# Kernel tuning notes

Measured on AMD Instinct MI355X. Metric: run time of the kernel, lower is better.

The kernel has to match this reference:

```python
import jax, jax.numpy as jnp
import numpy as np

DIM = 128
HEADS = 4
KV_RANK = 64
Q_RANK = 32
ROPE = DIM // 2   # 64
NOPE = DIM // 2   # 64
VDIM = DIM // 2   # 64
B, H, W = 2, 64, 64
EPS = 1e-5


def _conv1x1(x, w, b):
    # x: [B,C,H,W], w: [O,C], b: [O]
    return jnp.einsum('bchw,oc->bohw', x, w) + b[None, :, None, None]


def _gn1(x, g, b):
    # GroupNorm with 1 group: normalize over (C,H,W) per sample
    mu = jnp.mean(x, axis=(1, 2, 3), keepdims=True)
    var = jnp.mean((x - mu) ** 2, axis=(1, 2, 3), keepdims=True)
    return (x - mu) / jnp.sqrt(var + EPS) * g[None, :, None, None] + b[None, :, None, None]


def _freqs(h, w):
    # Replicates RotaryPositionalEncoding: pe[...,0::4]=sin_h, 1::4=cos_h, 2::4=sin_w, 3::4=cos_w
    n = ROPE // 4
    inv = 1.0 / (10000.0 ** (jnp.arange(n, dtype=jnp.float32) / n))
    ah = jnp.arange(h, dtype=jnp.float32)[:, None] * inv  # [h,n]
    aw = jnp.arange(w, dtype=jnp.float32)[:, None] * inv  # [w,n]
    fh = jnp.stack([jnp.sin(ah), jnp.cos(ah)], -1)  # [h,n,2] -> (real=sin_h, imag=cos_h)
    fw = jnp.stack([jnp.sin(aw), jnp.cos(aw)], -1)  # [w,n,2]
    fh_b = jnp.broadcast_to(fh[:, None], (h, w, n, 2))
    fw_b = jnp.broadcast_to(fw[None, :], (h, w, n, 2))
    # interleave pairs: pair 2m -> fh[m], pair 2m+1 -> fw[m]
    pe = jnp.stack([fh_b, fw_b], axis=3).reshape(h * w, ROPE // 2, 2)
    return pe  # [S, ROPE//2, 2]


def _rope(x, f):
    # x: [..., S, ROPE]; f: [S, ROPE//2, 2]
    xp = x.reshape(x.shape[:-1] + (ROPE // 2, 2))
    fr, fi = f[..., 0], f[..., 1]  # [S, ROPE//2] broadcast over leading dims
    rr = xp[..., 0] * fr - xp[..., 1] * fi
    ri = xp[..., 0] * fi + xp[..., 1] * fr
    return jnp.stack([rr, ri], -1).reshape(x.shape)


def setup_inputs() -> dict:
    key = jax.random.key(0)
    ks = jax.random.split(key, 8)
    s = 0.02
    inp = {
        'x': jax.random.normal(ks[0], (B, DIM, H, W), dtype=jnp.float32),
        'q1_w': jax.random.normal(ks[1], (Q_RANK, DIM), dtype=jnp.float32) * s,
        'q1_b': jnp.zeros((Q_RANK,), jnp.float32),
        'q_gn_g': jnp.ones((Q_RANK,), jnp.float32),
        'q_gn_b': jnp.zeros((Q_RANK,), jnp.float32),
        'q2_w': jax.random.normal(ks[2], (HEADS * (NOPE + ROPE), Q_RANK), dtype=jnp.float32) * s,
        'q2_b': jnp.zeros((HEADS * (NOPE + ROPE),), jnp.float32),
        'kv1_w': jax.random.normal(ks[3], (KV_RANK + ROPE, DIM), dtype=jnp.float32) * s,
        'kv1_b': jnp.zeros((KV_RANK + ROPE,), jnp.float32),
        'kv_gn_g': jnp.ones((KV_RANK + ROPE,), jnp.float32),
        'kv_gn_b': jnp.zeros((KV_RANK + ROPE,), jnp.float32),
        'kvn_g': jnp.ones((KV_RANK,), jnp.float32),
        'kvn_b': jnp.zeros((KV_RANK,), jnp.float32),
        'kvup_w': jax.random.normal(ks[4], (HEADS * (NOPE + VDIM), KV_RANK), dtype=jnp.float32) * s,
        'kvup_b': jnp.zeros((HEADS * (NOPE + VDIM),), jnp.float32),
        'out_w': jax.random.normal(ks[5], (DIM, HEADS * VDIM), dtype=jnp.float32) * s,
        'out_b': jnp.zeros((DIM,), jnp.float32),
    }
    return inp


def reference(x, q1_w, q1_b, q_gn_g, q_gn_b, q2_w, q2_b, kv1_w, kv1_b, kv_gn_g, kv_gn_b, kvn_g, kvn_b, kvup_w, kvup_b, out_w, out_b):
    b, c, h, w = x.shape
    s = h * w
    f = _freqs(h, w)  # [S, ROPE//2, 2]

    # Q path: low-rank down -> GN -> up
    q = _conv1x1(_gn1(_conv1x1(x, q1_w, q1_b), q_gn_g, q_gn_b), q2_w, q2_b)
    q = q.reshape(b, HEADS, NOPE + ROPE, s).transpose(0, 1, 3, 2)  # [B,H,S,D]
    q_nope, q_rope = q[..., :NOPE], q[..., NOPE:]
    q = jnp.concatenate([q_nope, _rope(q_rope, f)], axis=-1)

    # KV path: joint down-proj, split rope-k and compressed kv
    kv = _gn1(_conv1x1(x, kv1_w, kv1_b), kv_gn_g, kv_gn_b)  # [B, ROPE+KV_RANK, H, W]
    k_rope_c, kv_c = kv[:, :ROPE], kv[:, ROPE:]
    kv_u = _conv1x1(_gn1(kv_c, kvn_g, kvn_b), kvup_w, kvup_b)
    kv_u = kv_u.reshape(b, HEADS, NOPE + VDIM, s).transpose(0, 1, 3, 2)
    k_nope, v = kv_u[..., :NOPE], kv_u[..., NOPE:]

    k_rope = _rope(k_rope_c.reshape(b, ROPE, s).transpose(0, 2, 1)[:, None], f)  # [B,1,S,ROPE]
    k = jnp.concatenate([k_nope, jnp.broadcast_to(k_rope, (b, HEADS, s, ROPE))], axis=-1)

    scale = (NOPE + ROPE) ** -0.5
    attn = jax.nn.softmax(jnp.einsum('bhqd,bhkd->bhqk', q, k) * scale, axis=-1)
    o = jnp.einsum('bhqk,bhkd->bhqd', attn, v)  # [B,H,S,VDIM]
    o = o.transpose(0, 1, 3, 2).reshape(b, HEADS * VDIM, h, w)
    return _conv1x1(o, out_w, out_b) + x
```

## Files before the change

kernel.cpp:

```cpp
#include <hip/hip_runtime.h>

typedef unsigned short ushort_t;
typedef unsigned int uint_t;
typedef __attribute__((ext_vector_type(8))) short s16x8;
typedef __attribute__((ext_vector_type(4))) short s16x4;
typedef __attribute__((ext_vector_type(4))) float f32x4;
typedef __attribute__((ext_vector_type(16))) float f32x16;

#define S_TOT 4096
#define QSCALE 0.08838834764831845f
#define LOG2E 1.4426950408889634f
#define QSL (QSCALE * LOG2E)
#define L2_10000_D16 0.8304820237218406f

__device__ __forceinline__ ushort_t f2b(float f) {
  uint_t u = __float_as_uint(f);
  uint_t r = (u + 0x7FFFu + ((u >> 16) & 1u)) >> 16;
  return (ushort_t)r;
}

__device__ __forceinline__ float b2f(ushort_t u) {
  return __uint_as_float((uint_t)u << 16);
}

__device__ __forceinline__ uint_t cvt_pk_bf16(float lo, float hi) {
  uint_t r;
  asm("v_cvt_pk_bf16_f32 %0, %1, %2" : "=v"(r) : "v"(lo), "v"(hi));
  return r;
}

__device__ __forceinline__ void gload16(const void* g, void* l) {
  __builtin_amdgcn_global_load_lds(
      (const __attribute__((address_space(1))) unsigned int*)g,
      (__attribute__((address_space(3))) unsigned int*)l, 16, 0, 0);
}

__device__ __forceinline__ void rope_pair(float& x0, float& x1, int p, int hi, int wi, float scale) {
  float inv = exp2f(-(float)(p >> 1) * L2_10000_D16);
  float ang = ((p & 1) ? (float)wi : (float)hi) * inv;
  float sn = sinf(ang), cs = cosf(ang);
  float r0 = (x0 * sn - x1 * cs) * scale;
  float r1 = (x0 * cs + x1 * sn) * scale;
  x0 = r0; x1 = r1;
}

__global__ __launch_bounds__(256) void k_conv1(
    const float* __restrict__ x, const float* __restrict__ q1_w, const float* __restrict__ q1_b,
    const float* __restrict__ kv1_w, const float* __restrict__ kv1_b,
    float* __restrict__ y_q, float* __restrict__ y_kv, double* __restrict__ pch,
    const float* __restrict__ q2_w, const float* __restrict__ kvup_w,
    const float* __restrict__ out_w, ushort_t* __restrict__ wq2,
    ushort_t* __restrict__ wkvup, ushort_t* __restrict__ wout) {
  if (blockIdx.x >= 512) {
    int i = (blockIdx.x - 512) * 256 + threadIdx.x;
    if (i < 16384) wq2[i] = f2b(q2_w[i]);
    else if (i < 49152) wkvup[i - 16384] = f2b(kvup_w[i - 16384]);
    else if (i < 81920) wout[i - 49152] = f2b(out_w[i - 49152]);
    return;
  }
  const int b = blockIdx.x >> 8, blk = blockIdx.x & 255, st = blk * 16;
  const int t = threadIdx.x, si = t & 15, g = t >> 4;
  __shared__ float xs[128][16];
#pragma unroll
  for (int i = 0; i < 8; i++) {
    int c = g + 16 * i;
    xs[c][si] = x[(size_t)(b * 128 + c) * S_TOT + st + si];
  }
  __syncthreads();
  float acc[10];
#pragma unroll
  for (int i = 0; i < 10; i++) {
    int oc = g * 10 + i;
    acc[i] = (oc < 32) ? q1_b[oc] : kv1_b[oc - 32];
  }
  const float4* q1w4 = (const float4*)q1_w;
  const float4* kv1w4 = (const float4*)kv1_w;
  for (int c4 = 0; c4 < 32; c4++) {
    float x0 = xs[c4 * 4 + 0][si], x1 = xs[c4 * 4 + 1][si];
    float x2 = xs[c4 * 4 + 2][si], x3 = xs[c4 * 4 + 3][si];
#pragma unroll
    for (int i = 0; i < 10; i++) {
      int oc = g * 10 + i;
      float4 wv = (oc < 32) ? q1w4[oc * 32 + c4] : kv1w4[(oc - 32) * 32 + c4];
      acc[i] += wv.x * x0 + wv.y * x1 + wv.z * x2 + wv.w * x3;
    }
  }
  double* pbase = pch + (size_t)(b * 256 + blk) * 320;
#pragma unroll
  for (int i = 0; i < 10; i++) {
    int oc = g * 10 + i;
    float a = acc[i];
    if (oc < 32) y_q[(size_t)(b * 32 + oc) * S_TOT + st + si] = a;
    else         y_kv[(size_t)(b * 128 + oc - 32) * S_TOT + st + si] = a;
    double s = a, q = (double)a * a;
#pragma unroll
    for (int o = 1; o < 16; o <<= 1) { s += __shfl_xor(s, o, 16); q += __shfl_xor(q, o, 16); }
    if (si == 0) { pbase[oc * 2] = s; pbase[oc * 2 + 1] = q; }
  }
}

__global__ __launch_bounds__(256) void k_red(
    const double* __restrict__ pch, double* __restrict__ SQ) {
  const int pair = blockIdx.x;
  const int b = pair / 160, c = pair % 160;
  const int tid = threadIdx.x;
  __shared__ double rs[256], rq[256];
  rs[tid] = pch[(size_t)(b * 256 + tid) * 320 + c * 2];
  rq[tid] = pch[(size_t)(b * 256 + tid) * 320 + c * 2 + 1];
  __syncthreads();
#pragma unroll
  for (int o = 128; o > 0; o >>= 1) {
    if (tid < o) { rs[tid] += rs[tid + o]; rq[tid] += rq[tid + o]; }
    __syncthreads();
  }
  if (tid == 0) { SQ[pair * 2] = rs[0]; SQ[pair * 2 + 1] = rq[0]; }
}

__global__ __launch_bounds__(512) void k_stats(
    const double* __restrict__ SQ,
    const float* __restrict__ qg, const float* __restrict__ qb,
    const float* __restrict__ kvg, const float* __restrict__ kvb,
    const float* __restrict__ kng, const float* __restrict__ knb,
    float* __restrict__ coef) {
  __shared__ double Sh[2][160], Qh[2][160];
  const int tid = threadIdx.x;
  if (tid < 320) {
    int b = tid / 160, c = tid % 160;
    Sh[b][c] = SQ[tid * 2]; Qh[b][c] = SQ[tid * 2 + 1];
  }
  __syncthreads();
  if (tid < 2) {
    int b = tid;
    float* cf = coef + b * 320;
    const double NS = 4096.0;
    double muq = 0, m2q = 0;
    for (int c = 0; c < 32; c++) { muq += Sh[b][c]; m2q += Qh[b][c]; }
    muq /= (32.0 * NS); m2q /= (32.0 * NS);
    double rstdq = 1.0 / sqrt(m2q - muq * muq + 1e-5);
    for (int c = 0; c < 32; c++) {
      double A = rstdq * (double)qg[c];
      cf[c] = (float)A; cf[32 + c] = (float)((double)qb[c] - muq * A);
    }
    double mukv = 0, m2kv = 0;
    for (int c = 0; c < 128; c++) { mukv += Sh[b][32 + c]; m2kv += Qh[b][32 + c]; }
    mukv /= (128.0 * NS); m2kv /= (128.0 * NS);
    double rstdkv = 1.0 / sqrt(m2kv - mukv * mukv + 1e-5);
    for (int c = 0; c < 64; c++) {
      double A = rstdkv * (double)kvg[c];
      cf[64 + c] = (float)A; cf[128 + c] = (float)((double)kvb[c] - mukv * A);
    }
    double mu2 = 0, m22 = 0;
    for (int c2 = 0; c2 < 64; c2++) {
      int c = 64 + c2;
      double a = rstdkv * (double)kvg[c], bb = (double)kvb[c] - mukv * a;
      double Ec = Sh[b][32 + c] / NS, M2c = Qh[b][32 + c] / NS;
      mu2 += a * Ec + bb;
      m22 += a * a * M2c + 2.0 * a * bb * Ec + bb * bb;
    }
    mu2 /= 64.0; m22 /= 64.0;
    double rstd2 = 1.0 / sqrt(m22 - mu2 * mu2 + 1e-5);
    for (int c2 = 0; c2 < 64; c2++) {
      int c = 64 + c2;
      double a = rstdkv * (double)kvg[c], bb = (double)kvb[c] - mukv * a;
      cf[192 + c2] = (float)(a * rstd2 * (double)kng[c2]);
      cf[256 + c2] = (float)((bb - mu2) * rstd2 * (double)kng[c2] + (double)knb[c2]);
    }
  }
}

__global__ __launch_bounds__(256) void k_gq(
    const float* __restrict__ y_q, const float* __restrict__ coef,
    const ushort_t* __restrict__ wq2, const float* __restrict__ q2_b,
    ushort_t* __restrict__ Q) {
  const int id = blockIdx.x;
  const int h = id & 3, st = (id >> 2) & 63, b = id >> 8;
  const int t = threadIdx.x, si = t & 63, wid = t >> 6;
  const int l15 = t & 15, lg = (t >> 4) & 3;
  const float* cf = coef + b * 320;
  __shared__ __align__(16) ushort_t Xt[64][64];
  __shared__ __align__(16) ushort_t sQ[64][128];
  {
    ushort_t pk[8];
#pragma unroll
    for (int j = 0; j < 8; j++) {
      int c = wid * 8 + j;
      float v = y_q[(size_t)(b * 32 + c) * S_TOT + st * 64 + si];
      pk[j] = f2b(v * cf[c] + cf[32 + c]);
    }
    *(s16x8*)((char*)&Xt[si][0] + ((wid * 16) ^ ((si & 7) << 4))) = *(s16x8*)pk;
  }
  __syncthreads();
  const int d0w = wid * 32;
  f32x4 acc[2][4];
#pragma unroll
  for (int db = 0; db < 2; db++) {
    f32x4 bv;
#pragma unroll
    for (int r = 0; r < 4; r++) bv[r] = q2_b[h * 128 + d0w + db * 16 + lg * 4 + r];
#pragma unroll
    for (int sb = 0; sb < 4; sb++) acc[db][sb] = bv;
  }
  s16x8 wf[2];
#pragma unroll
  for (int db = 0; db < 2; db++)
    wf[db] = *(const s16x8*)(wq2 + (size_t)(h * 128 + d0w + db * 16 + l15) * 32 + lg * 8);
  const int xsw = (lg * 16) ^ ((l15 & 7) << 4);
#pragma unroll
  for (int sb = 0; sb < 4; sb++) {
    s16x8 xf = *(const s16x8*)((const char*)&Xt[sb * 16 + l15][0] + xsw);
#pragma unroll
    for (int db = 0; db < 2; db++)
      acc[db][sb] = __builtin_amdgcn_mfma_f32_16x16x32_bf16(wf[db], xf, acc[db][sb], 0, 0, 0);
  }
  if (wid >= 2) {
#pragma unroll
    for (int db = 0; db < 2; db++)
#pragma unroll
      for (int sb = 0; sb < 4; sb++) {
        int sp = st * 64 + sb * 16 + l15, hi = sp >> 6, wi = sp & 63;
        int dg = d0w + db * 16 + lg * 4;
#pragma unroll
        for (int pr = 0; pr < 2; pr++) {
          float v0 = acc[db][sb][pr * 2], v1 = acc[db][sb][pr * 2 + 1];
          int p = (dg + pr * 2 - 64) >> 1;
          rope_pair(v0, v1, p, hi, wi, QSL);
          acc[db][sb][pr * 2] = v0; acc[db][sb][pr * 2 + 1] = v1;
        }
      }
  } else {
#pragma unroll
    for (int db = 0; db < 2; db++)
#pragma unroll
      for (int sb = 0; sb < 4; sb++)
#pragma unroll
        for (int r = 0; r < 4; r++) acc[db][sb][r] *= QSL;
  }
#pragma unroll
  for (int db = 0; db < 2; db++)
#pragma unroll
    for (int sb = 0; sb < 4; sb++) {
      ushort_t pk[4];
#pragma unroll
      for (int r = 0; r < 4; r++) pk[r] = f2b(acc[db][sb][r]);
      int srow = sb * 16 + l15;
      *(s16x4*)((char*)&sQ[srow][0] + (((d0w + db * 16 + lg * 4) * 2) ^ ((srow & 7) << 4))) =
          *(s16x4*)pk;
    }
  __syncthreads();
  ushort_t* qrow = Q + ((size_t)(b * 4 + h) * S_TOT + st * 64 + si) * 128 + wid * 32;
#pragma unroll
  for (int j = 0; j < 4; j++) {
    s16x8 v = *(const s16x8*)((const char*)&sQ[si][0] + ((wid * 64 + j * 16) ^ ((si & 7) << 4)));
    *(s16x8*)(qrow + j * 8) = v;
  }
}

__global__ __launch_bounds__(256) void k_gkv(
    const float* __restrict__ y_kv, const float* __restrict__ coef,
    const ushort_t* __restrict__ wkvup, const float* __restrict__ kvup_b,
    ushort_t* __restrict__ K, ushort_t* __restrict__ VT) {
  const int id = blockIdx.x;
  const int h = id & 3, st = (id >> 2) & 63, b = id >> 8;
  const int t = threadIdx.x, si = t & 63, wid = t >> 6;
  const int l15 = t & 15, lg = (t >> 4) & 3;
  const float* cf = coef + b * 320;
  __shared__ __align__(16) ushort_t Xt[64][64];
  __shared__ __align__(16) ushort_t sK[64][64];
  {
#pragma unroll
    for (int half = 0; half < 2; half++) {
      ushort_t pk[8];
#pragma unroll
      for (int j = 0; j < 8; j++) {
        int c2 = wid * 16 + half * 8 + j;
        float v = y_kv[(size_t)(b * 128 + 64 + c2) * S_TOT + st * 64 + si];
        pk[j] = f2b(v * cf[192 + c2] + cf[256 + c2]);
      }
      *(s16x8*)((char*)&Xt[si][0] + ((wid * 32 + half * 16) ^ ((si & 7) << 4))) = *(s16x8*)pk;
    }
  }
  __syncthreads();
  const int d0w = wid * 32;
  f32x4 acc[2][4];
#pragma unroll
  for (int db = 0; db < 2; db++) {
    f32x4 bv;
#pragma unroll
    for (int r = 0; r < 4; r++) bv[r] = kvup_b[h * 128 + d0w + db * 16 + lg * 4 + r];
#pragma unroll
    for (int sb = 0; sb < 4; sb++) acc[db][sb] = bv;
  }
  s16x8 wf[2][2];
#pragma unroll
  for (int db = 0; db < 2; db++)
#pragma unroll
    for (int kk = 0; kk < 2; kk++)
      wf[db][kk] = *(const s16x8*)(wkvup + (size_t)(h * 128 + d0w + db * 16 + l15) * 64 +
                                   kk * 32 + lg * 8);
#pragma unroll
  for (int sb = 0; sb < 4; sb++) {
#pragma unroll
    for (int kk = 0; kk < 2; kk++) {
      s16x8 xf = *(const s16x8*)((const char*)&Xt[sb * 16 + l15][0] +
                                 ((kk * 64 + lg * 16) ^ ((l15 & 7) << 4)));
#pragma unroll
      for (int db = 0; db < 2; db++)
        acc[db][sb] = __builtin_amdgcn_mfma_f32_16x16x32_bf16(wf[db][kk], xf, acc[db][sb], 0, 0, 0);
    }
  }
  if (wid < 2) {
#pragma unroll
    for (int db = 0; db < 2; db++)
#pragma unroll
      for (int sb = 0; sb < 4; sb++) {
        ushort_t pk[4];
#pragma unroll
        for (int r = 0; r < 4; r++) pk[r] = f2b(acc[db][sb][r]);
        int srow = sb * 16 + l15;
        *(s16x4*)((char*)&sK[srow][0] + (((d0w + db * 16 + lg * 4) * 2) ^ ((srow & 7) << 4))) =
            *(s16x4*)pk;
      }
  } else {
    ushort_t* vb = VT + (size_t)(b * 4 + h) * 64 * S_TOT;
#pragma unroll
    for (int db = 0; db < 2; db++)
#pragma unroll
      for (int sb = 0; sb < 4; sb++) {
        int sp = st * 64 + sb * 16 + l15;
#pragma unroll
        for (int r = 0; r < 4; r++) {
          int vd = (wid - 2) * 32 + db * 16 + lg * 4 + r;
          vb[(size_t)vd * S_TOT + sp] = f2b(acc[db][sb][r]);
        }
      }
  }
  __syncthreads();
  const int sp = st * 64 + si;
  ushort_t* krow = K + ((size_t)(b * 4 + h) * S_TOT + sp) * 128;
#pragma unroll
  for (int j = 0; j < 2; j++) {
    s16x8 v = *(const s16x8*)((const char*)&sK[si][0] + ((wid * 32 + j * 16) ^ ((si & 7) << 4)));
    *(s16x8*)(krow + wid * 16 + j * 8) = v;
  }
  {
    const int c0 = wid * 16, hi = sp >> 6, wi = sp & 63;
    float v[16];
#pragma unroll
    for (int j = 0; j < 16; j++) {
      int c = c0 + j;
      v[j] = y_kv[(size_t)(b * 128 + c) * S_TOT + sp] * cf[64 + c] + cf[128 + c];
    }
#pragma unroll
    for (int k = 0; k < 8; k++) {
      int p = (c0 >> 1) + k;
      rope_pair(v[2 * k], v[2 * k + 1], p, hi, wi, 1.0f);
    }
    ushort_t pk[16];
#pragma unroll
    for (int j = 0; j < 16; j++) pk[j] = f2b(v[j]);
    *(s16x8*)(krow + 64 + c0) = *(s16x8*)pk;
    *(s16x8*)(krow + 64 + c0 + 8) = *(s16x8*)(pk + 8);
  }
}

__global__ __launch_bounds__(256, 3) void k_attn(
    const ushort_t* __restrict__ Q, const ushort_t* __restrict__ K,
    const ushort_t* __restrict__ VT, ushort_t* __restrict__ Opart,
    float* __restrict__ ml) {
  const int bid = blockIdx.x;
  const int bh = bid & 7;
  const int rest = bid >> 3;
  const int half = rest >> 5, qblk = rest & 31;
  const int kv0 = half * 2048;
  const int tid = threadIdx.x;
  const int wid = tid >> 6, lane = tid & 63;
  const int l31 = lane & 31, hi = lane >> 5;
  const int qbase = qblk * 128 + wid * 32;
  const ushort_t* Qp = Q + (size_t)bh * S_TOT * 128;
  const ushort_t* Kp = K + (size_t)bh * S_TOT * 128;
  const ushort_t* Vp = VT + (size_t)bh * 64 * S_TOT;

  __shared__ __align__(16) ushort_t K_lds[2][64][128];
  __shared__ __align__(16) ushort_t V_lds[2][64][64];

  s16x8 qf[8];
#pragma unroll
  for (int c = 0; c < 8; c++)
    qf[c] = *(const s16x8*)(Qp + (size_t)(qbase + l31) * 128 + c * 16 + hi * 8);

  f32x16 o0, o1;
#pragma unroll
  for (int r = 0; r < 16; r++) { o0[r] = 0.f; o1[r] = 0.f; }
  float m_s = -1e30f, l_s = 0.f;

  const int krow_l = tid >> 4;
  const int kcolb = (tid & 15) * 16;
  const int vrow_l = tid >> 3;
  const int vcolb = (tid & 7) * 16;

#define STAGE(kvb, bufi)                                                          \
  {                                                                               \
    _Pragma("unroll")                                                             \
    for (int i = 0; i < 4; i++) {                                                 \
      int row = i * 16 + krow_l;                                                  \
      int colb = kcolb ^ ((row & 15) << 4);                                       \
      gload16((const char*)(Kp + (size_t)((kvb) + row) * 128) + colb,             \
              (void*)&K_lds[bufi][i * 16 + wid * 4][0]);                          \
    }                                                                             \
    _Pragma("unroll")                                                             \
    for (int i = 0; i < 2; i++) {                                                 \
      int vd = i * 32 + vrow_l;                                                   \
      int colb = vcolb ^ ((vd & 7) << 4);                                         \
      gload16((const char*)(Vp + (size_t)vd * S_TOT + (kvb)) + colb,              \
              (void*)&V_lds[bufi][i * 32 + wid * 8][0]);                          \
    }                                                                             \
  }

  STAGE(kv0, 0);
  __syncthreads();

  const int kswz = (l31 & 15) << 4;
  const int vswz = (l31 & 7) << 4;
#pragma unroll 1
  for (int t = 0; t < 32; t++) {
    const int buf = t & 1;
    if (t < 31) STAGE(kv0 + (t + 1) * 64, buf ^ 1);
    f32x16 sc0, sc1;
#pragma unroll
    for (int r = 0; r < 16; r++) { sc0[r] = 0.f; sc1[r] = 0.f; }
    __builtin_amdgcn_s_setprio(1);
#pragma unroll
    for (int c = 0; c < 8; c++) {
      const int off = (c * 32 + hi * 16) ^ kswz;
      s16x8 k0 = *(const s16x8*)((const char*)&K_lds[buf][l31][0] + off);
      s16x8 k1 = *(const s16x8*)((const char*)&K_lds[buf][32 + l31][0] + off);
      sc0 = __builtin_amdgcn_mfma_f32_32x32x16_bf16(k0, qf[c], sc0, 0, 0, 0);
      sc1 = __builtin_amdgcn_mfma_f32_32x32x16_bf16(k1, qf[c], sc1, 0, 0, 0);
    }
    __builtin_amdgcn_s_setprio(0);
    float pmax;
    {
      float a = fmaxf(sc0[0], sc0[1]);
#pragma unroll
      for (int r = 2; r < 16; r++) a = fmaxf(a, sc0[r]);
#pragma unroll
      for (int r = 0; r < 16; r++) a = fmaxf(a, sc1[r]);
      pmax = a;
    }
    pmax = fmaxf(pmax, __shfl_xor(pmax, 32, 64));
    if (__any(pmax - m_s > 11.5f)) {
      float mn = fmaxf(m_s, pmax);
      float alpha = exp2f(m_s - mn);
      m_s = mn;
      l_s *= alpha;
#pragma unroll
      for (int r = 0; r < 16; r++) { o0[r] *= alpha; o1[r] *= alpha; }
    }
    float rs = 0.f;
#pragma unroll
    for (int r = 0; r < 16; r++) {
      float p0 = exp2f(sc0[r] - m_s);
      float p1 = exp2f(sc1[r] - m_s);
      sc0[r] = p0; sc1[r] = p1;
      rs += p0 + p1;
    }
    l_s += rs;
    __builtin_amdgcn_s_setprio(1);
#pragma unroll
    for (int c = 0; c < 4; c++) {
      const f32x16 P = (c < 2) ? sc0 : sc1;
      const int rA = 8 * (c & 1);
      uint_t a0 = cvt_pk_bf16(P[rA + 0], P[rA + 1]);
      uint_t a1 = cvt_pk_bf16(P[rA + 2], P[rA + 3]);
      uint_t b0 = cvt_pk_bf16(P[rA + 4], P[rA + 5]);
      uint_t b1 = cvt_pk_bf16(P[rA + 6], P[rA + 7]);
      uint_t s0 = hi ? a0 : b0, s1 = hi ? a1 : b1;
      uint_t r0 = (uint_t)__shfl_xor((int)s0, 32, 64);
      uint_t r1 = (uint_t)__shfl_xor((int)s1, 32, 64);
      union { uint_t u[4]; s16x8 v; } pf;
      pf.u[0] = hi ? r0 : a0; pf.u[1] = hi ? r1 : a1;
      pf.u[2] = hi ? b0 : r0; pf.u[3] = hi ? b1 : r1;
      const int voff = (c * 32 + hi * 16) ^ vswz;
      s16x8 v0 = *(const s16x8*)((const char*)&V_lds[buf][l31][0] + voff);
      s16x8 v1 = *(const s16x8*)((const char*)&V_lds[buf][32 + l31][0] + voff);
      o0 = __builtin_amdgcn_mfma_f32_32x32x16_bf16(v0, pf.v, o0, 0, 0, 0);
      o1 = __builtin_amdgcn_mfma_f32_32x32x16_bf16(v1, pf.v, o1, 0, 0, 0);
    }
    __builtin_amdgcn_s_setprio(0);
    __syncthreads();
  }
#undef STAGE
  l_s += __shfl_xor(l_s, 32, 64);
  float linv = 1.f / l_s;
  if (lane < 32) {
    float* mlrow = ml + ((size_t)(half * 8 + bh) * S_TOT + qbase + l31) * 2;
    mlrow[0] = m_s; mlrow[1] = l_s;
  }
  char* sO = (char*)&K_lds[0][0][0];
#pragma unroll
  for (int vt = 0; vt < 2; vt++) {
#pragma unroll
    for (int r = 0; r < 16; r += 2) {
      float v0 = (vt ? o1[r] : o0[r]) * linv;
      float v1 = (vt ? o1[r + 1] : o0[r + 1]) * linv;
      uint_t u = cvt_pk_bf16(v0, v1);
      int vd = vt * 32 + (r & 3) + 8 * (r >> 2) + 4 * hi;
      *(uint_t*)(sO + (wid * 32 + l31) * 128 + ((vd * 2) ^ ((l31 & 7) << 4))) = u;
    }
  }
  __syncthreads();
  {
    const int r = tid >> 1, hf = tid & 1;
    const int w = r >> 5, ql = r & 31;
    ushort_t* orow = Opart + ((size_t)(half * 8 + bh) * S_TOT + qblk * 128 + r) * 64 + hf * 32;
#pragma unroll
    for (int j = 0; j < 4; j++) {
      s16x8 v = *(const s16x8*)(sO + (w * 32 + ql) * 128 + ((hf * 64 + j * 16) ^ ((ql & 7) << 4)));
      *(s16x8*)(orow + j * 8) = v;
    }
  }
}

__global__ __launch_bounds__(256) void k_oc(
    const ushort_t* __restrict__ Opart, const float* __restrict__ ml,
    const ushort_t* __restrict__ wout, const float* __restrict__ out_b,
    const float* __restrict__ x, float* __restrict__ out) {
  const int id = blockIdx.x;
  const int cch = id & 1, st32 = (id >> 1) & 127, b = id >> 8;
  const int t = threadIdx.x, wid = t >> 6;
  const int l15 = t & 15, lg = (t >> 4) & 3;
  __shared__ __align__(16) ushort_t Xt[32][256];
  {
    const int s = t & 31, grp = t >> 5;
    const int h = grp >> 1, vd0 = (grp & 1) * 32;
    const int sp = st32 * 32 + s;
    const float2 ml0 = *(const float2*)&ml[((size_t)(b * 4 + h) * S_TOT + sp) * 2];
    const float2 ml1 = *(const float2*)&ml[((size_t)(8 + b * 4 + h) * S_TOT + sp) * 2];
    float mm = fmaxf(ml0.x, ml1.x);
    float w0 = exp2f(ml0.x - mm) * ml0.y, w1 = exp2f(ml1.x - mm) * ml1.y;
    float inv = 1.f / (w0 + w1);
    w0 *= inv; w1 *= inv;
    const ushort_t* oa = Opart + ((size_t)(b * 4 + h) * S_TOT + sp) * 64 + vd0;
    const ushort_t* obp = oa + (size_t)8 * S_TOT * 64;
#pragma unroll
    for (int j4 = 0; j4 < 4; j4++) {
      union { s16x8 v; ushort_t u[8]; } av, bv2;
      av.v = *(const s16x8*)(oa + j4 * 8);
      bv2.v = *(const s16x8*)(obp + j4 * 8);
      ushort_t pk[8];
#pragma unroll
      for (int j = 0; j < 8; j++) pk[j] = f2b(w0 * b2f(av.u[j]) + w1 * b2f(bv2.u[j]));
      *(s16x8*)((char*)&Xt[s][0] + ((grp * 64 + j4 * 16) ^ ((s & 7) << 4))) = *(s16x8*)pk;
    }
  }
  __syncthreads();
  const int c0w = cch * 64 + wid * 16;
  f32x4 acc[2];
  {
    f32x4 bv;
#pragma unroll
    for (int r = 0; r < 4; r++) bv[r] = out_b[c0w + lg * 4 + r];
    acc[0] = bv; acc[1] = bv;
  }
#pragma unroll
  for (int kk = 0; kk < 8; kk++) {
    s16x8 wf = *(const s16x8*)(wout + (size_t)(c0w + l15) * 256 + kk * 32 + lg * 8);
#pragma unroll
    for (int sb = 0; sb < 2; sb++) {
      s16x8 xf = *(const s16x8*)((const char*)&Xt[sb * 16 + l15][0] +
                                 ((kk * 64 + lg * 16) ^ ((l15 & 7) << 4)));
      acc[sb] = __builtin_amdgcn_mfma_f32_16x16x32_bf16(wf, xf, acc[sb], 0, 0, 0);
    }
  }
#pragma unroll
  for (int sb = 0; sb < 2; sb++) {
#pragma unroll
    for (int r = 0; r < 4; r++) {
      int c = c0w + lg * 4 + r;
      int sp = st32 * 32 + sb * 16 + l15;
      size_t idx = (size_t)(b * 128 + c) * S_TOT + sp;
      out[idx] = acc[sb][r] + x[idx];
    }
  }
}

extern "C" void kernel_launch(void* const* d_in, const int* in_sizes, int n_in,
                              void* d_out, int out_size, void* d_ws, size_t ws_size,
                              hipStream_t stream) {
  const float* x      = (const float*)d_in[0];
  const float* q1_w   = (const float*)d_in[1];
  const float* q1_b   = (const float*)d_in[2];
  const float* q_gn_g = (const float*)d_in[3];
  const float* q_gn_b = (const float*)d_in[4];
  const float* q2_w   = (const float*)d_in[5];
  const float* q2_b   = (const float*)d_in[6];
  const float* kv1_w  = (const float*)d_in[7];
  const float* kv1_b  = (const float*)d_in[8];
  const float* kv_gn_g= (const float*)d_in[9];
  const float* kv_gn_b= (const float*)d_in[10];
  const float* kvn_g  = (const float*)d_in[11];
  const float* kvn_b  = (const float*)d_in[12];
  const float* kvup_w = (const float*)d_in[13];
  const float* kvup_b = (const float*)d_in[14];
  const float* out_w  = (const float*)d_in[15];
  const float* out_b  = (const float*)d_in[16];

  const size_t MB = 1u << 20;
  char* ws = (char*)d_ws;
  float*    y_q   = (float*)(ws);
  float*    y_kv  = (float*)(ws + 1 * MB);
  ushort_t* Q     = (ushort_t*)(ws + 5 * MB);
  ushort_t* K     = (ushort_t*)(ws + 13 * MB);
  ushort_t* VT    = (ushort_t*)(ws + 21 * MB);
  double*   pch   = (double*)(ws + 25 * MB);
  float*    coef  = (float*)(ws + 27 * MB);
  ushort_t* wq2   = (ushort_t*)(ws + 27 * MB + 65536);
  ushort_t* wkvup = (ushort_t*)(ws + 27 * MB + 131072);
  ushort_t* wout  = (ushort_t*)(ws + 27 * MB + 262144);
  double*   SQ    = (double*)(ws + 27 * MB + 524288);
  ushort_t* Opart = (ushort_t*)(ws + 29 * MB);
  float*    ml    = (float*)(ws + 38 * MB);
  float*    out   = (float*)d_out;

  k_conv1<<<832, 256, 0, stream>>>(x, q1_w, q1_b, kv1_w, kv1_b, y_q, y_kv, pch,
                                   q2_w, kvup_w, out_w, wq2, wkvup, wout);
  k_red  <<<320, 256, 0, stream>>>(pch, SQ);
  k_stats<<<1,   512, 0, stream>>>(SQ, q_gn_g, q_gn_b, kv_gn_g, kv_gn_b, kvn_g, kvn_b, coef);
  k_gq   <<<512, 256, 0, stream>>>(y_q, coef, wq2, q2_b, Q);
  k_gkv  <<<512, 256, 0, stream>>>(y_kv, coef, wkvup, kvup_b, K, VT);
  k_attn <<<512, 256, 0, stream>>>(Q, K, VT, Opart, ml);
  k_oc   <<<512, 256, 0, stream>>>(Opart, ml, wout, out_b, x, out);
}
```

Before: 152.5 us.

## Split attention KV range into four parts and use finer-grained barriers

```diff
diff --git a/kernel.cpp b/kernel.cpp
--- a/kernel.cpp
+++ b/kernel.cpp
@@ -370,8 +370,8 @@
   const int bid = blockIdx.x;
   const int bh = bid & 7;
   const int rest = bid >> 3;
-  const int half = rest >> 5, qblk = rest & 31;
-  const int kv0 = half * 2048;
+  const int part = rest >> 5, qblk = rest & 31;
+  const int kv0 = part * 1024;
   const int tid = threadIdx.x;
   const int wid = tid >> 6, lane = tid & 63;
   const int l31 = lane & 31, hi = lane >> 5;
@@ -417,14 +417,20 @@
   }
 
   STAGE(kv0, 0);
-  __syncthreads();
 
   const int kswz = (l31 & 15) << 4;
   const int vswz = (l31 & 7) << 4;
 #pragma unroll 1
-  for (int t = 0; t < 32; t++) {
+  for (int t = 0; t < 16; t++) {
     const int buf = t & 1;
-    if (t < 31) STAGE(kv0 + (t + 1) * 64, buf ^ 1);
+    if (t < 15) {
+      STAGE(kv0 + (t + 1) * 64, buf ^ 1);
+      asm volatile("s_waitcnt vmcnt(6)" ::: "memory");
+    } else {
+      asm volatile("s_waitcnt vmcnt(0)" ::: "memory");
+    }
+    __builtin_amdgcn_s_barrier();
+    __builtin_amdgcn_sched_barrier(0);
     f32x16 sc0, sc1;
 #pragma unroll
     for (int r = 0; r < 16; r++) { sc0[r] = 0.f; sc1[r] = 0.f; }
@@ -487,13 +493,14 @@
       o1 = __builtin_amdgcn_mfma_f32_32x32x16_bf16(v1, pf.v, o1, 0, 0, 0);
     }
     __builtin_amdgcn_s_setprio(0);
-    __syncthreads();
+    __builtin_amdgcn_sched_barrier(0);
+    __builtin_amdgcn_s_barrier();
   }
 #undef STAGE
   l_s += __shfl_xor(l_s, 32, 64);
   float linv = 1.f / l_s;
   if (lane < 32) {
-    float* mlrow = ml + ((size_t)(half * 8 + bh) * S_TOT + qbase + l31) * 2;
+    float* mlrow = ml + ((size_t)(part * 8 + bh) * S_TOT + qbase + l31) * 2;
     mlrow[0] = m_s; mlrow[1] = l_s;
   }
   char* sO = (char*)&K_lds[0][0][0];
@@ -512,7 +519,7 @@
   {
     const int r = tid >> 1, hf = tid & 1;
     const int w = r >> 5, ql = r & 31;
-    ushort_t* orow = Opart + ((size_t)(half * 8 + bh) * S_TOT + qblk * 128 + r) * 64 + hf * 32;
+    ushort_t* orow = Opart + ((size_t)(part * 8 + bh) * S_TOT + qblk * 128 + r) * 64 + hf * 32;
 #pragma unroll
     for (int j = 0; j < 4; j++) {
       s16x8 v = *(const s16x8*)(sO + (w * 32 + ql) * 128 + ((hf * 64 + j * 16) ^ ((ql & 7) << 4)));
@@ -534,22 +541,33 @@
     const int s = t & 31, grp = t >> 5;
     const int h = grp >> 1, vd0 = (grp & 1) * 32;
     const int sp = st32 * 32 + s;
-    const float2 ml0 = *(const float2*)&ml[((size_t)(b * 4 + h) * S_TOT + sp) * 2];
-    const float2 ml1 = *(const float2*)&ml[((size_t)(8 + b * 4 + h) * S_TOT + sp) * 2];
-    float mm = fmaxf(ml0.x, ml1.x);
-    float w0 = exp2f(ml0.x - mm) * ml0.y, w1 = exp2f(ml1.x - mm) * ml1.y;
-    float inv = 1.f / (w0 + w1);
-    w0 *= inv; w1 *= inv;
-    const ushort_t* oa = Opart + ((size_t)(b * 4 + h) * S_TOT + sp) * 64 + vd0;
-    const ushort_t* obp = oa + (size_t)8 * S_TOT * 64;
+    const int bh = b * 4 + h;
+    float2 mlp[4];
+#pragma unroll
+    for (int p = 0; p < 4; p++)
+      mlp[p] = *(const float2*)&ml[((size_t)(p * 8 + bh) * S_TOT + sp) * 2];
+    float mm = fmaxf(fmaxf(mlp[0].x, mlp[1].x), fmaxf(mlp[2].x, mlp[3].x));
+    float w[4], wsum = 0.f;
+#pragma unroll
+    for (int p = 0; p < 4; p++) { w[p] = exp2f(mlp[p].x - mm) * mlp[p].y; wsum += w[p]; }
+    float inv = 1.f / wsum;
+#pragma unroll
+    for (int p = 0; p < 4; p++) w[p] *= inv;
 #pragma unroll
     for (int j4 = 0; j4 < 4; j4++) {
-      union { s16x8 v; ushort_t u[8]; } av, bv2;
-      av.v = *(const s16x8*)(oa + j4 * 8);
-      bv2.v = *(const s16x8*)(obp + j4 * 8);
+      float accv[8];
+#pragma unroll
+      for (int j = 0; j < 8; j++) accv[j] = 0.f;
+#pragma unroll
+      for (int p = 0; p < 4; p++) {
+        union { s16x8 v; ushort_t u[8]; } av;
+        av.v = *(const s16x8*)(Opart + ((size_t)(p * 8 + bh) * S_TOT + sp) * 64 + vd0 + j4 * 8);
+#pragma unroll
+        for (int j = 0; j < 8; j++) accv[j] += w[p] * b2f(av.u[j]);
+      }
       ushort_t pk[8];
 #pragma unroll
-      for (int j = 0; j < 8; j++) pk[j] = f2b(w0 * b2f(av.u[j]) + w1 * b2f(bv2.u[j]));
+      for (int j = 0; j < 8; j++) pk[j] = f2b(accv[j]);
       *(s16x8*)((char*)&Xt[s][0] + ((grp * 64 + j4 * 16) ^ ((s & 7) << 4))) = *(s16x8*)pk;
     }
   }
@@ -613,21 +631,21 @@
   ushort_t* K     = (ushort_t*)(ws + 13 * MB);
   ushort_t* VT    = (ushort_t*)(ws + 21 * MB);
   double*   pch   = (double*)(ws + 25 * MB);
-  float*    coef  = (float*)(ws + 27 * MB);
-  ushort_t* wq2   = (ushort_t*)(ws + 27 * MB + 65536);
-  ushort_t* wkvup = (ushort_t*)(ws + 27 * MB + 131072);
-  ushort_t* wout  = (ushort_t*)(ws + 27 * MB + 262144);
-  double*   SQ    = (double*)(ws + 27 * MB + 524288);
-  ushort_t* Opart = (ushort_t*)(ws + 29 * MB);
-  float*    ml    = (float*)(ws + 38 * MB);
+  double*   SQ    = (double*)(ws + 26 * MB + 524288);
+  float*    coef  = (float*)(ws + 26 * MB + 532480);
+  ushort_t* wq2   = (ushort_t*)(ws + 26 * MB + 540672);
+  ushort_t* wkvup = (ushort_t*)(ws + 26 * MB + 573440);
+  ushort_t* wout  = (ushort_t*)(ws + 26 * MB + 638976);
+  ushort_t* Opart = (ushort_t*)(ws + 27 * MB);
+  float*    ml    = (float*)(ws + 43 * MB);
   float*    out   = (float*)d_out;
 
-  k_conv1<<<832, 256, 0, stream>>>(x, q1_w, q1_b, kv1_w, kv1_b, y_q, y_kv, pch,
-                                   q2_w, kvup_w, out_w, wq2, wkvup, wout);
-  k_red  <<<320, 256, 0, stream>>>(pch, SQ);
-  k_stats<<<1,   512, 0, stream>>>(SQ, q_gn_g, q_gn_b, kv_gn_g, kv_gn_b, kvn_g, kvn_b, coef);
-  k_gq   <<<512, 256, 0, stream>>>(y_q, coef, wq2, q2_b, Q);
-  k_gkv  <<<512, 256, 0, stream>>>(y_kv, coef, wkvup, kvup_b, K, VT);
-  k_attn <<<512, 256, 0, stream>>>(Q, K, VT, Opart, ml);
-  k_oc   <<<512, 256, 0, stream>>>(Opart, ml, wout, out_b, x, out);
-}
+  k_conv1<<<832,  256, 0, stream>>>(x, q1_w, q1_b, kv1_w, kv1_b, y_q, y_kv, pch,
+                                    q2_w, kvup_w, out_w, wq2, wkvup, wout);
+  k_red  <<<320,  256, 0, stream>>>(pch, SQ);
+  k_stats<<<1,    512, 0, stream>>>(SQ, q_gn_g, q_gn_b, kv_gn_g, kv_gn_b, kvn_g, kvn_b, coef);
+  k_gq   <<<512,  256, 0, stream>>>(y_q, coef, wq2, q2_b, Q);
+  k_gkv  <<<512,  256, 0, stream>>>(y_kv, coef, wkvup, kvup_b, K, VT);
+  k_attn <<<1024, 256, 0, stream>>>(Q, K, VT, Opart, ml);
+  k_oc   <<<512,  256, 0, stream>>>(Opart, ml, wout, out_b, x, out);
+}
```

New measurement: 161.2 us. +5.7%, slower.

## Merge GN reduction kernels, fuse Q/KV builders, relax attention barriers

Applied to the files above, without the earlier changes.

```diff
diff --git a/kernel.cpp b/kernel.cpp
--- a/kernel.cpp
+++ b/kernel.cpp
@@ -85,7 +85,6 @@
       acc[i] += wv.x * x0 + wv.y * x1 + wv.z * x2 + wv.w * x3;
     }
   }
-  double* pbase = pch + (size_t)(b * 256 + blk) * 320;
 #pragma unroll
   for (int i = 0; i < 10; i++) {
     int oc = g * 10 + i;
@@ -95,38 +94,29 @@
     double s = a, q = (double)a * a;
 #pragma unroll
     for (int o = 1; o < 16; o <<= 1) { s += __shfl_xor(s, o, 16); q += __shfl_xor(q, o, 16); }
-    if (si == 0) { pbase[oc * 2] = s; pbase[oc * 2 + 1] = q; }
-  }
-}
-
-__global__ __launch_bounds__(256) void k_red(
-    const double* __restrict__ pch, double* __restrict__ SQ) {
-  const int pair = blockIdx.x;
-  const int b = pair / 160, c = pair % 160;
-  const int tid = threadIdx.x;
-  __shared__ double rs[256], rq[256];
-  rs[tid] = pch[(size_t)(b * 256 + tid) * 320 + c * 2];
-  rq[tid] = pch[(size_t)(b * 256 + tid) * 320 + c * 2 + 1];
-  __syncthreads();
-#pragma unroll
-  for (int o = 128; o > 0; o >>= 1) {
-    if (tid < o) { rs[tid] += rs[tid + o]; rq[tid] += rq[tid + o]; }
-    __syncthreads();
-  }
-  if (tid == 0) { SQ[pair * 2] = rs[0]; SQ[pair * 2 + 1] = rq[0]; }
-}
-
-__global__ __launch_bounds__(512) void k_stats(
-    const double* __restrict__ SQ,
+    if (si == 0) {
+      double* pt = pch + (size_t)(b * 160 + oc) * 512 + blk * 2;
+      pt[0] = s; pt[1] = q;
+    }
+  }
+}
+
+__global__ __launch_bounds__(1024) void k_redstats(
+    const double* __restrict__ pch,
     const float* __restrict__ qg, const float* __restrict__ qb,
     const float* __restrict__ kvg, const float* __restrict__ kvb,
     const float* __restrict__ kng, const float* __restrict__ knb,
     float* __restrict__ coef) {
   __shared__ double Sh[2][160], Qh[2][160];
-  const int tid = threadIdx.x;
-  if (tid < 320) {
-    int b = tid / 160, c = tid % 160;
-    Sh[b][c] = SQ[tid * 2]; Qh[b][c] = SQ[tid * 2 + 1];
+  const int tid = threadIdx.x, w = tid >> 6, lane = tid & 63;
+  for (int pair = w; pair < 320; pair += 16) {
+    const double* p = pch + (size_t)pair * 512 + lane * 8;
+    double s = 0, q = 0;
+#pragma unroll
+    for (int j = 0; j < 4; j++) { s += p[j * 2]; q += p[j * 2 + 1]; }
+#pragma unroll
+    for (int o = 1; o < 64; o <<= 1) { s += __shfl_xor(s, o, 64); q += __shfl_xor(q, o, 64); }
+    if (lane == 0) { Sh[pair / 160][pair % 160] = s; Qh[pair / 160][pair % 160] = q; }
   }
   __syncthreads();
   if (tid < 2) {
@@ -168,17 +158,17 @@
   }
 }
 
-__global__ __launch_bounds__(256) void k_gq(
+__device__ __forceinline__ void gq_body(
+    int id, ushort_t* smem,
     const float* __restrict__ y_q, const float* __restrict__ coef,
     const ushort_t* __restrict__ wq2, const float* __restrict__ q2_b,
     ushort_t* __restrict__ Q) {
-  const int id = blockIdx.x;
   const int h = id & 3, st = (id >> 2) & 63, b = id >> 8;
   const int t = threadIdx.x, si = t & 63, wid = t >> 6;
   const int l15 = t & 15, lg = (t >> 4) & 3;
   const float* cf = coef + b * 320;
-  __shared__ __align__(16) ushort_t Xt[64][64];
-  __shared__ __align__(16) ushort_t sQ[64][128];
+  ushort_t* Xt = smem;
+  ushort_t* sQ = smem + 4096;
   {
     ushort_t pk[8];
 #pragma unroll
@@ -187,7 +177,7 @@
       float v = y_q[(size_t)(b * 32 + c) * S_TOT + st * 64 + si];
       pk[j] = f2b(v * cf[c] + cf[32 + c]);
     }
-    *(s16x8*)((char*)&Xt[si][0] + ((wid * 16) ^ ((si & 7) << 4))) = *(s16x8*)pk;
+    *(s16x8*)((char*)(Xt + si * 64) + ((wid * 16) ^ ((si & 7) << 4))) = *(s16x8*)pk;
   }
   __syncthreads();
   const int d0w = wid * 32;
@@ -207,7 +197,7 @@
   const int xsw = (lg * 16) ^ ((l15 & 7) << 4);
 #pragma unroll
   for (int sb = 0; sb < 4; sb++) {
-    s16x8 xf = *(const s16x8*)((const char*)&Xt[sb * 16 + l15][0] + xsw);
+    s16x8 xf = *(const s16x8*)((const char*)(Xt + (sb * 16 + l15) * 64) + xsw);
 #pragma unroll
     for (int db = 0; db < 2; db++)
       acc[db][sb] = __builtin_amdgcn_mfma_f32_16x16x32_bf16(wf[db], xf, acc[db][sb], 0, 0, 0);
@@ -243,29 +233,29 @@
 #pragma unroll
       for (int r = 0; r < 4; r++) pk[r] = f2b(acc[db][sb][r]);
       int srow = sb * 16 + l15;
-      *(s16x4*)((char*)&sQ[srow][0] + (((d0w + db * 16 + lg * 4) * 2) ^ ((srow & 7) << 4))) =
+      *(s16x4*)((char*)(sQ + srow * 128) + (((d0w + db * 16 + lg * 4) * 2) ^ ((srow & 7) << 4))) =
           *(s16x4*)pk;
     }
   __syncthreads();
   ushort_t* qrow = Q + ((size_t)(b * 4 + h) * S_TOT + st * 64 + si) * 128 + wid * 32;
 #pragma unroll
   for (int j = 0; j < 4; j++) {
-    s16x8 v = *(const s16x8*)((const char*)&sQ[si][0] + ((wid * 64 + j * 16) ^ ((si & 7) << 4)));
+    s16x8 v = *(const s16x8*)((const char*)(sQ + si * 128) + ((wid * 64 + j * 16) ^ ((si & 7) << 4)));
     *(s16x8*)(qrow + j * 8) = v;
   }
 }
 
-__global__ __launch_bounds__(256) void k_gkv(
+__device__ __forceinline__ void gkv_body(
+    int id, ushort_t* smem,
     const float* __restrict__ y_kv, const float* __restrict__ coef,
     const ushort_t* __restrict__ wkvup, const float* __restrict__ kvup_b,
     ushort_t* __restrict__ K, ushort_t* __restrict__ VT) {
-  const int id = blockIdx.x;
   const int h = id & 3, st = (id >> 2) & 63, b = id >> 8;
   const int t = threadIdx.x, si = t & 63, wid = t >> 6;
   const int l15 = t & 15, lg = (t >> 4) & 3;
   const float* cf = coef + b * 320;
-  __shared__ __align__(16) ushort_t Xt[64][64];
-  __shared__ __align__(16) ushort_t sK[64][64];
+  ushort_t* Xt = smem;
+  ushort_t* sK = smem + 4096;
   {
 #pragma unroll
     for (int half = 0; half < 2; half++) {
@@ -276,7 +266,7 @@
         float v = y_kv[(size_t)(b * 128 + 64 + c2) * S_TOT + st * 64 + si];
         pk[j] = f2b(v * cf[192 + c2] + cf[256 + c2]);
       }
-      *(s16x8*)((char*)&Xt[si][0] + ((wid * 32 + half * 16) ^ ((si & 7) << 4))) = *(s16x8*)pk;
+      *(s16x8*)((char*)(Xt + si * 64) + ((wid * 32 + half * 16) ^ ((si & 7) << 4))) = *(s16x8*)pk;
     }
   }
   __syncthreads();
@@ -301,7 +291,7 @@
   for (int sb = 0; sb < 4; sb++) {
 #pragma unroll
     for (int kk = 0; kk < 2; kk++) {
-      s16x8 xf = *(const s16x8*)((const char*)&Xt[sb * 16 + l15][0] +
+      s16x8 xf = *(const s16x8*)((const char*)(Xt + (sb * 16 + l15) * 64) +
                                  ((kk * 64 + lg * 16) ^ ((l15 & 7) << 4)));
 #pragma unroll
       for (int db = 0; db < 2; db++)
@@ -317,7 +307,7 @@
 #pragma unroll
         for (int r = 0; r < 4; r++) pk[r] = f2b(acc[db][sb][r]);
         int srow = sb * 16 + l15;
-        *(s16x4*)((char*)&sK[srow][0] + (((d0w + db * 16 + lg * 4) * 2) ^ ((srow & 7) << 4))) =
+        *(s16x4*)((char*)(sK + srow * 64) + (((d0w + db * 16 + lg * 4) * 2) ^ ((srow & 7) << 4))) =
             *(s16x4*)pk;
       }
   } else {
@@ -339,7 +329,7 @@
   ushort_t* krow = K + ((size_t)(b * 4 + h) * S_TOT + sp) * 128;
 #pragma unroll
   for (int j = 0; j < 2; j++) {
-    s16x8 v = *(const s16x8*)((const char*)&sK[si][0] + ((wid * 32 + j * 16) ^ ((si & 7) << 4)));
+    s16x8 v = *(const s16x8*)((const char*)(sK + si * 64) + ((wid * 32 + j * 16) ^ ((si & 7) << 4)));
     *(s16x8*)(krow + wid * 16 + j * 8) = v;
   }
   {
@@ -361,6 +351,17 @@
     *(s16x8*)(krow + 64 + c0) = *(s16x8*)pk;
     *(s16x8*)(krow + 64 + c0 + 8) = *(s16x8*)(pk + 8);
   }
+}
+
+__global__ __launch_bounds__(256) void k_build(
+    const float* __restrict__ y_q, const float* __restrict__ y_kv,
+    const float* __restrict__ coef,
+    const ushort_t* __restrict__ wq2, const float* __restrict__ q2_b,
+    const ushort_t* __restrict__ wkvup, const float* __restrict__ kvup_b,
+    ushort_t* __restrict__ Q, ushort_t* __restrict__ K, ushort_t* __restrict__ VT) {
+  __shared__ __align__(16) ushort_t smem[12288];
+  if (blockIdx.x < 512) gq_body(blockIdx.x, smem, y_q, coef, wq2, q2_b, Q);
+  else                  gkv_body(blockIdx.x - 512, smem, y_kv, coef, wkvup, kvup_b, K, VT);
 }
 
 __global__ __launch_bounds__(256, 3) void k_attn(
@@ -417,14 +418,20 @@
   }
 
   STAGE(kv0, 0);
-  __syncthreads();
 
   const int kswz = (l31 & 15) << 4;
   const int vswz = (l31 & 7) << 4;
 #pragma unroll 1
   for (int t = 0; t < 32; t++) {
     const int buf = t & 1;
-    if (t < 31) STAGE(kv0 + (t + 1) * 64, buf ^ 1);
+    if (t < 31) {
+      STAGE(kv0 + (t + 1) * 64, buf ^ 1);
+      asm volatile("s_waitcnt vmcnt(6)" ::: "memory");
+    } else {
+      asm volatile("s_waitcnt vmcnt(0)" ::: "memory");
+    }
+    __builtin_amdgcn_s_barrier();
+    __builtin_amdgcn_sched_barrier(0);
     f32x16 sc0, sc1;
 #pragma unroll
     for (int r = 0; r < 16; r++) { sc0[r] = 0.f; sc1[r] = 0.f; }
@@ -487,7 +494,8 @@
       o1 = __builtin_amdgcn_mfma_f32_32x32x16_bf16(v1, pf.v, o1, 0, 0, 0);
     }
     __builtin_amdgcn_s_setprio(0);
-    __syncthreads();
+    __builtin_amdgcn_sched_barrier(0);
+    __builtin_amdgcn_s_barrier();
   }
 #undef STAGE
   l_s += __shfl_xor(l_s, 32, 64);
@@ -613,21 +621,19 @@
   ushort_t* K     = (ushort_t*)(ws + 13 * MB);
   ushort_t* VT    = (ushort_t*)(ws + 21 * MB);
   double*   pch   = (double*)(ws + 25 * MB);
-  float*    coef  = (float*)(ws + 27 * MB);
-  ushort_t* wq2   = (ushort_t*)(ws + 27 * MB + 65536);
-  ushort_t* wkvup = (ushort_t*)(ws + 27 * MB + 131072);
-  ushort_t* wout  = (ushort_t*)(ws + 27 * MB + 262144);
-  double*   SQ    = (double*)(ws + 27 * MB + 524288);
-  ushort_t* Opart = (ushort_t*)(ws + 29 * MB);
-  float*    ml    = (float*)(ws + 38 * MB);
+  float*    coef  = (float*)(ws + 26 * MB + 524288);
+  ushort_t* wq2   = (ushort_t*)(ws + 26 * MB + 540672);
+  ushort_t* wkvup = (ushort_t*)(ws + 26 * MB + 573440);
+  ushort_t* wout  = (ushort_t*)(ws + 26 * MB + 638976);
+  ushort_t* Opart = (ushort_t*)(ws + 27 * MB);
+  float*    ml    = (float*)(ws + 36 * MB);
   float*    out   = (float*)d_out;
 
-  k_conv1<<<832, 256, 0, stream>>>(x, q1_w, q1_b, kv1_w, kv1_b, y_q, y_kv, pch,
-                                   q2_w, kvup_w, out_w, wq2, wkvup, wout);
-  k_red  <<<320, 256, 0, stream>>>(pch, SQ);
-  k_stats<<<1,   512, 0, stream>>>(SQ, q_gn_g, q_gn_b, kv_gn_g, kv_gn_b, kvn_g, kvn_b, coef);
-  k_gq   <<<512, 256, 0, stream>>>(y_q, coef, wq2, q2_b, Q);
-  k_gkv  <<<512, 256, 0, stream>>>(y_kv, coef, wkvup, kvup_b, K, VT);
-  k_attn <<<512, 256, 0, stream>>>(Q, K, VT, Opart, ml);
-  k_oc   <<<512, 256, 0, stream>>>(Opart, ml, wout, out_b, x, out);
-}
+  k_conv1   <<<832,  256, 0, stream>>>(x, q1_w, q1_b, kv1_w, kv1_b, y_q, y_kv, pch,
+                                       q2_w, kvup_w, out_w, wq2, wkvup, wout);
+  k_redstats<<<1,   1024, 0, stream>>>(pch, q_gn_g, q_gn_b, kv_gn_g, kv_gn_b,
+                                       kvn_g, kvn_b, coef);
+  k_build   <<<1024, 256, 0, stream>>>(y_q, y_kv, coef, wq2, q2_b, wkvup, kvup_b, Q, K, VT);
+  k_attn    <<<512,  256, 0, stream>>>(Q, K, VT, Opart, ml);
+  k_oc      <<<512,  256, 0, stream>>>(Opart, ml, wout, out_b, x, out);
+}
```

New measurement: 168.5 us. 10.5% more time.

## Triple-buffer attention K/V staging and transpose GN partial-sum layout

Applied to the files above, without the earlier changes.

```diff
diff --git a/kernel.cpp b/kernel.cpp
--- a/kernel.cpp
+++ b/kernel.cpp
@@ -85,7 +85,6 @@
       acc[i] += wv.x * x0 + wv.y * x1 + wv.z * x2 + wv.w * x3;
     }
   }
-  double* pbase = pch + (size_t)(b * 256 + blk) * 320;
 #pragma unroll
   for (int i = 0; i < 10; i++) {
     int oc = g * 10 + i;
@@ -95,25 +94,28 @@
     double s = a, q = (double)a * a;
 #pragma unroll
     for (int o = 1; o < 16; o <<= 1) { s += __shfl_xor(s, o, 16); q += __shfl_xor(q, o, 16); }
-    if (si == 0) { pbase[oc * 2] = s; pbase[oc * 2 + 1] = q; }
+    if (si == 0) {
+      double* pt = pch + (size_t)(b * 160 + oc) * 512 + blk * 2;
+      pt[0] = s; pt[1] = q;
+    }
   }
 }
 
 __global__ __launch_bounds__(256) void k_red(
     const double* __restrict__ pch, double* __restrict__ SQ) {
-  const int pair = blockIdx.x;
-  const int b = pair / 160, c = pair % 160;
-  const int tid = threadIdx.x;
-  __shared__ double rs[256], rq[256];
-  rs[tid] = pch[(size_t)(b * 256 + tid) * 320 + c * 2];
-  rq[tid] = pch[(size_t)(b * 256 + tid) * 320 + c * 2 + 1];
-  __syncthreads();
-#pragma unroll
-  for (int o = 128; o > 0; o >>= 1) {
-    if (tid < o) { rs[tid] += rs[tid + o]; rq[tid] += rq[tid + o]; }
-    __syncthreads();
-  }
-  if (tid == 0) { SQ[pair * 2] = rs[0]; SQ[pair * 2 + 1] = rq[0]; }
+  const int pair = blockIdx.x, tid = threadIdx.x;
+  const int lane = tid & 63, wid = tid >> 6;
+  const double* p = pch + (size_t)pair * 512;
+  double s = p[tid * 2], q = p[tid * 2 + 1];
+#pragma unroll
+  for (int o = 1; o < 64; o <<= 1) { s += __shfl_xor(s, o, 64); q += __shfl_xor(q, o, 64); }
+  __shared__ double red[4][2];
+  if (lane == 0) { red[wid][0] = s; red[wid][1] = q; }
+  __syncthreads();
+  if (tid == 0) {
+    SQ[pair * 2]     = red[0][0] + red[1][0] + red[2][0] + red[3][0];
+    SQ[pair * 2 + 1] = red[0][1] + red[1][1] + red[2][1] + red[3][1];
+  }
 }
 
 __global__ __launch_bounds__(512) void k_stats(
@@ -363,7 +365,7 @@
   }
 }
 
-__global__ __launch_bounds__(256, 3) void k_attn(
+__global__ __launch_bounds__(256, 2) void k_attn(
     const ushort_t* __restrict__ Q, const ushort_t* __restrict__ K,
     const ushort_t* __restrict__ VT, ushort_t* __restrict__ Opart,
     float* __restrict__ ml) {
@@ -380,8 +382,8 @@
   const ushort_t* Kp = K + (size_t)bh * S_TOT * 128;
   const ushort_t* Vp = VT + (size_t)bh * 64 * S_TOT;
 
-  __shared__ __align__(16) ushort_t K_lds[2][64][128];
-  __shared__ __align__(16) ushort_t V_lds[2][64][64];
+  __shared__ __align__(16) ushort_t K_lds[3][64][128];
+  __shared__ __align__(16) ushort_t V_lds[3][64][64];
 
   s16x8 qf[8];
 #pragma unroll
@@ -417,14 +419,22 @@
   }
 
   STAGE(kv0, 0);
-  __syncthreads();
+  STAGE(kv0 + 64, 1);
 
   const int kswz = (l31 & 15) << 4;
   const int vswz = (l31 & 7) << 4;
 #pragma unroll 1
   for (int t = 0; t < 32; t++) {
-    const int buf = t & 1;
-    if (t < 31) STAGE(kv0 + (t + 1) * 64, buf ^ 1);
+    const int buf = t % 3;
+    if (t < 31) {
+      asm volatile("s_waitcnt vmcnt(6)" ::: "memory");
+    } else {
+      asm volatile("s_waitcnt vmcnt(0)" ::: "memory");
+    }
+    __builtin_amdgcn_sched_barrier(0);
+    __builtin_amdgcn_s_barrier();
+    __builtin_amdgcn_sched_barrier(0);
+    if (t < 30) STAGE(kv0 + (t + 2) * 64, (t + 2) % 3);
     f32x16 sc0, sc1;
 #pragma unroll
     for (int r = 0; r < 16; r++) { sc0[r] = 0.f; sc1[r] = 0.f; }
@@ -487,7 +497,6 @@
       o1 = __builtin_amdgcn_mfma_f32_32x32x16_bf16(v1, pf.v, o1, 0, 0, 0);
     }
     __builtin_amdgcn_s_setprio(0);
-    __syncthreads();
   }
 #undef STAGE
   l_s += __shfl_xor(l_s, 32, 64);
@@ -613,13 +622,13 @@
   ushort_t* K     = (ushort_t*)(ws + 13 * MB);
   ushort_t* VT    = (ushort_t*)(ws + 21 * MB);
   double*   pch   = (double*)(ws + 25 * MB);
-  float*    coef  = (float*)(ws + 27 * MB);
-  ushort_t* wq2   = (ushort_t*)(ws + 27 * MB + 65536);
-  ushort_t* wkvup = (ushort_t*)(ws + 27 * MB + 131072);
-  ushort_t* wout  = (ushort_t*)(ws + 27 * MB + 262144);
-  double*   SQ    = (double*)(ws + 27 * MB + 524288);
-  ushort_t* Opart = (ushort_t*)(ws + 29 * MB);
-  float*    ml    = (float*)(ws + 38 * MB);
+  double*   SQ    = (double*)(ws + 26 * MB + 524288);
+  float*    coef  = (float*)(ws + 26 * MB + 532480);
+  ushort_t* wq2   = (ushort_t*)(ws + 26 * MB + 540672);
+  ushort_t* wkvup = (ushort_t*)(ws + 26 * MB + 573440);
+  ushort_t* wout  = (ushort_t*)(ws + 26 * MB + 638976);
+  ushort_t* Opart = (ushort_t*)(ws + 27 * MB);
+  float*    ml    = (float*)(ws + 36 * MB);
   float*    out   = (float*)d_out;
 
   k_conv1<<<832, 256, 0, stream>>>(x, q1_w, q1_b, kv1_w, kv1_b, y_q, y_kv, pch,
```

Result: no change. 152.4 us (-0.1%).
